# Kernel optimization log

Hardware: AMD Instinct MI355X
Metric: run time of the kernel (lower is better)

## Reference

```python
import jax, jax.numpy as jnp
import numpy as np

B, C, N = 4, 64, 512
H = 128  # hidden width; MLP input is 2*C = 128


def setup_inputs() -> dict:
    key = jax.random.key(0)
    k0, k1, k2 = jax.random.split(key, 3)
    x = jax.random.normal(k0, (B, C, N), dtype=jnp.float32)
    # Torch Linear init ~ U(-1/sqrt(fan_in), 1/sqrt(fan_in)); stored as (in, out) for einsum.
    W1 = jax.random.normal(k1, (2 * C, H), dtype=jnp.float32) * (1.0 / np.sqrt(2 * C))
    b1 = jnp.zeros((H,), dtype=jnp.float32)
    W2 = jax.random.normal(k2, (H, 1), dtype=jnp.float32) * (1.0 / np.sqrt(H))
    b2 = jnp.zeros((1,), dtype=jnp.float32)
    return {"x": x, "W1": W1, "b1": b1, "W2": W2, "b2": b2}


def reference(x, W1, b1, W2, b2):
    # x: (B, C, N). Equivalent to the per-offset loop: for every pair (i, j) with
    # j > i, score = MLP(concat(x[:, :, i], x[:, :, j])), placed at y[:, i, j].
    # Dropout is identity in eval mode.
    b, c, n = x.shape
    xt = jnp.transpose(x, (0, 2, 1))                      # (B, N, C)
    left = jnp.broadcast_to(xt[:, :, None, :], (b, n, n, c))   # row index i
    right = jnp.broadcast_to(xt[:, None, :, :], (b, n, n, c))  # col index j
    pairs = jnp.concatenate([left, right], axis=-1)       # (B, N, N, 2C)
    h = jax.nn.relu(jnp.einsum('bijc,ch->bijh', pairs, W1) + b1)
    score = (jnp.einsum('bijh,ho->bijo', h, W2) + b2)[..., 0]  # (B, N, N)
    mask = jnp.triu(jnp.ones((n, n), dtype=score.dtype), k=1)  # strict upper triangle
    return score * mask
```

## Files before the change

kernel.cpp:

```cpp
#include <hip/hip_runtime.h>

#define B_ 4
#define C_ 64
#define N_ 512
#define H_ 128

__global__ __launch_bounds__(256) void proj_kernel(
    const float* __restrict__ x, const float* __restrict__ W1,
    const float* __restrict__ b1, float* __restrict__ Lbuf,
    float* __restrict__ Rbuf)
{
    __shared__ float Wl[64 * 128];
    __shared__ float xs[16 * 68];

    const int t    = threadIdx.x;
    const int half = blockIdx.x >> 7;
    const int rem  = blockIdx.x & 127;
    const int b    = rem >> 5;
    const int i0   = (rem & 31) * 16;
    const int cbase = half * 64;

    const float4* W14 = (const float4*)W1;
    float4* Wl4 = (float4*)Wl;
    #pragma unroll
    for (int k = 0; k < 8; ++k)
        Wl4[t + k * 256] = W14[cbase * 32 + t + k * 256];

    #pragma unroll
    for (int k = 0; k < 4; ++k) {
        int idx = t + k * 256;
        int c = idx >> 4, ii = idx & 15;
        xs[ii * 68 + c] = x[b * (C_ * N_) + c * N_ + i0 + ii];
    }
    __syncthreads();

    const int hq  = t & 31;
    const int il  = (t >> 5) * 2;
    const int col = hq * 4;

    float4 a0, a1;
    if (half) { a0 = *(const float4*)(b1 + col); a1 = a0; }
    else      { a0 = make_float4(0.f, 0.f, 0.f, 0.f); a1 = a0; }

    #pragma unroll
    for (int c = 0; c < 64; c += 4) {
        float4 xv0 = *(float4*)(xs + il * 68 + c);
        float4 xv1 = *(float4*)(xs + (il + 1) * 68 + c);
        const float* x0p = (const float*)&xv0;
        const float* x1p = (const float*)&xv1;
        #pragma unroll
        for (int cc = 0; cc < 4; ++cc) {
            float4 w = Wl4[(c + cc) * 32 + hq];
            a0.x = fmaf(w.x, x0p[cc], a0.x);
            a0.y = fmaf(w.y, x0p[cc], a0.y);
            a0.z = fmaf(w.z, x0p[cc], a0.z);
            a0.w = fmaf(w.w, x0p[cc], a0.w);
            a1.x = fmaf(w.x, x1p[cc], a1.x);
            a1.y = fmaf(w.y, x1p[cc], a1.y);
            a1.z = fmaf(w.z, x1p[cc], a1.z);
            a1.w = fmaf(w.w, x1p[cc], a1.w);
        }
    }

    float* buf = half ? Rbuf : Lbuf;
    float* o = buf + b * (N_ * H_) + (i0 + il) * H_ + col;
    *(float4*)o = a0;
    *(float4*)(o + H_) = a1;
}

__global__ __launch_bounds__(256) void pair_kernel(
    const float* __restrict__ Lbuf, const float* __restrict__ Rbuf,
    const float* __restrict__ W2, const float* __restrict__ b2,
    float* __restrict__ out)
{
    __shared__ float Lt[64 * 128];
    __shared__ float Rt[64 * 128];

    const int t    = threadIdx.x;
    const int b    = blockIdx.x >> 6;
    const int tile = blockIdx.x & 63;
    const int ti0  = (tile >> 3) * 64;
    const int tj0  = (tile & 7) * 64;

    float* outb = out + b * (N_ * N_);

    if (tj0 < ti0) {
        float4 z = make_float4(0.f, 0.f, 0.f, 0.f);
        #pragma unroll
        for (int k = 0; k < 4; ++k) {
            int idx4 = t + k * 256;
            int r = idx4 >> 4, cc = idx4 & 15;
            *(float4*)(outb + (ti0 + r) * N_ + tj0 + cc * 4) = z;
        }
        return;
    }

    float4* Lt4 = (float4*)Lt;
    float4* Rt4 = (float4*)Rt;
    #pragma unroll
    for (int k = 0; k < 8; ++k) {
        int idx4 = t + k * 256;
        int row = idx4 >> 5, hc = idx4 & 31;
        float4 lv = *(const float4*)(Lbuf + b * (N_ * H_) + (ti0 + row) * H_ + hc * 4);
        float4 rv = *(const float4*)(Rbuf + b * (N_ * H_) + (tj0 + row) * H_ + hc * 4);
        int sc = (hc + (row >> 2)) & 31;
        Lt4[row * 32 + sc] = lv;
        Rt4[row * 32 + sc] = rv;
    }
    __syncthreads();

    const int w    = t >> 6;
    const int lane = t & 63;
    const int wi   = (w >> 1) * 32, wj = (w & 1) * 32;
    const int til  = wi + ((lane >> 3) & 7) * 4;
    const int tjl  = wj + (lane & 7) * 4;
    const int rotL = til >> 2;
    const int rotR = tjl >> 2;

    float acc[4][4];
    #pragma unroll
    for (int r = 0; r < 4; ++r)
        #pragma unroll
        for (int c = 0; c < 4; ++c) acc[r][c] = 0.f;

    #pragma unroll 2
    for (int hc = 0; hc < 32; ++hc) {
        const int scL = (hc + rotL) & 31;
        const int scR = (hc + rotR) & 31;
        float4 Lr[4], Rc[4];
        #pragma unroll
        for (int r = 0; r < 4; ++r) Lr[r] = Lt4[(til + r) * 32 + scL];
        #pragma unroll
        for (int c = 0; c < 4; ++c) Rc[c] = Rt4[(tjl + c) * 32 + scR];
        float4 wv = *(const float4*)(W2 + hc * 4);
        const float* wp = (const float*)&wv;
        #pragma unroll
        for (int r = 0; r < 4; ++r) {
            const float* lp = (const float*)&Lr[r];
            #pragma unroll
            for (int c = 0; c < 4; ++c) {
                const float* rp = (const float*)&Rc[c];
                float s = acc[r][c];
                #pragma unroll
                for (int k = 0; k < 4; ++k) {
                    float v = fmaxf(lp[k] + rp[k], 0.f);
                    s = fmaf(v, wp[k], s);
                }
                acc[r][c] = s;
            }
        }
    }

    const float bias2 = b2[0];
    #pragma unroll
    for (int r = 0; r < 4; ++r) {
        const int gi = ti0 + til + r;
        float4 v;
        float* vp = (float*)&v;
        #pragma unroll
        for (int c = 0; c < 4; ++c) {
            const int gj = tj0 + tjl + c;
            vp[c] = (gj > gi) ? (acc[r][c] + bias2) : 0.f;
        }
        *(float4*)(outb + gi * N_ + tj0 + tjl) = v;
    }
}

extern "C" void kernel_launch(void* const* d_in, const int* in_sizes, int n_in,
                              void* d_out, int out_size, void* d_ws, size_t ws_size,
                              hipStream_t stream)
{
    const float* x  = (const float*)d_in[0];
    const float* W1 = (const float*)d_in[1];
    const float* b1 = (const float*)d_in[2];
    const float* W2 = (const float*)d_in[3];
    const float* b2 = (const float*)d_in[4];
    float* out  = (float*)d_out;
    float* Lbuf = (float*)d_ws;
    float* Rbuf = Lbuf + B_ * N_ * H_;

    proj_kernel<<<256, 256, 0, stream>>>(x, W1, b1, Lbuf, Rbuf);
    pair_kernel<<<B_ * 64, 256, 0, stream>>>(Lbuf, Rbuf, W2, b2, out);
}
```

Measured before the change: 80.41 us.

## Shrink pair kernel tiles to 32x32 with one-wave blocks and XOR swizzle

```diff
diff --git a/kernel.cpp b/kernel.cpp
--- a/kernel.cpp
+++ b/kernel.cpp
@@ -68,54 +68,48 @@
     *(float4*)(o + H_) = a1;
 }
 
-__global__ __launch_bounds__(256) void pair_kernel(
+__global__ __launch_bounds__(64) void pair_kernel(
     const float* __restrict__ Lbuf, const float* __restrict__ Rbuf,
     const float* __restrict__ W2, const float* __restrict__ b2,
     float* __restrict__ out)
 {
-    __shared__ float Lt[64 * 128];
-    __shared__ float Rt[64 * 128];
+    __shared__ float4 Lt4[32 * 32];
+    __shared__ float4 Rt4[32 * 32];
 
     const int t    = threadIdx.x;
-    const int b    = blockIdx.x >> 6;
-    const int tile = blockIdx.x & 63;
-    const int ti0  = (tile >> 3) * 64;
-    const int tj0  = (tile & 7) * 64;
+    const int b    = blockIdx.x >> 8;
+    const int tile = blockIdx.x & 255;
+    const int ti0  = (tile >> 4) * 32;
+    const int tj0  = (tile & 15) * 32;
 
     float* outb = out + b * (N_ * N_);
 
-    if (tj0 < ti0) {
+    if (tj0 + 31 <= ti0) {
         float4 z = make_float4(0.f, 0.f, 0.f, 0.f);
         #pragma unroll
         for (int k = 0; k < 4; ++k) {
-            int idx4 = t + k * 256;
-            int r = idx4 >> 4, cc = idx4 & 15;
-            *(float4*)(outb + (ti0 + r) * N_ + tj0 + cc * 4) = z;
+            int idx = t + k * 64;
+            int r = idx >> 3, cq = idx & 7;
+            *(float4*)(outb + (ti0 + r) * N_ + tj0 + cq * 4) = z;
         }
         return;
     }
 
-    float4* Lt4 = (float4*)Lt;
-    float4* Rt4 = (float4*)Rt;
+    const float* Lsrc = Lbuf + b * (N_ * H_) + ti0 * H_;
+    const float* Rsrc = Rbuf + b * (N_ * H_) + tj0 * H_;
     #pragma unroll
-    for (int k = 0; k < 8; ++k) {
-        int idx4 = t + k * 256;
-        int row = idx4 >> 5, hc = idx4 & 31;
-        float4 lv = *(const float4*)(Lbuf + b * (N_ * H_) + (ti0 + row) * H_ + hc * 4);
-        float4 rv = *(const float4*)(Rbuf + b * (N_ * H_) + (tj0 + row) * H_ + hc * 4);
-        int sc = (hc + (row >> 2)) & 31;
-        Lt4[row * 32 + sc] = lv;
-        Rt4[row * 32 + sc] = rv;
+    for (int k = 0; k < 16; ++k) {
+        int idx = t + k * 64;
+        int row = idx >> 5, hc = idx & 31;
+        int sc = hc ^ (row >> 2);
+        Lt4[row * 32 + sc] = *(const float4*)(Lsrc + idx * 4);
+        Rt4[row * 32 + sc] = *(const float4*)(Rsrc + idx * 4);
     }
     __syncthreads();
 
-    const int w    = t >> 6;
-    const int lane = t & 63;
-    const int wi   = (w >> 1) * 32, wj = (w & 1) * 32;
-    const int til  = wi + ((lane >> 3) & 7) * 4;
-    const int tjl  = wj + (lane & 7) * 4;
-    const int rotL = til >> 2;
-    const int rotR = tjl >> 2;
+    const int gL  = t >> 3;
+    const int gR  = t & 7;
+    const int til = gL * 4, tjl = gR * 4;
 
     float acc[4][4];
     #pragma unroll
@@ -123,16 +117,18 @@
         #pragma unroll
         for (int c = 0; c < 4; ++c) acc[r][c] = 0.f;
 
+    const float4* W24 = (const float4*)W2;
+
     #pragma unroll 2
     for (int hc = 0; hc < 32; ++hc) {
-        const int scL = (hc + rotL) & 31;
-        const int scR = (hc + rotR) & 31;
+        const int scL = hc ^ gL;
+        const int scR = hc ^ gR;
         float4 Lr[4], Rc[4];
         #pragma unroll
         for (int r = 0; r < 4; ++r) Lr[r] = Lt4[(til + r) * 32 + scL];
         #pragma unroll
         for (int c = 0; c < 4; ++c) Rc[c] = Rt4[(tjl + c) * 32 + scR];
-        float4 wv = *(const float4*)(W2 + hc * 4);
+        float4 wv = W24[hc];
         const float* wp = (const float*)&wv;
         #pragma unroll
         for (int r = 0; r < 4; ++r) {
@@ -180,5 +176,5 @@
     float* Rbuf = Lbuf + B_ * N_ * H_;
 
     proj_kernel<<<256, 256, 0, stream>>>(x, W1, b1, Lbuf, Rbuf);
-    pair_kernel<<<B_ * 64, 256, 0, stream>>>(Lbuf, Rbuf, W2, b2, out);
+    pair_kernel<<<B_ * 256, 64, 0, stream>>>(Lbuf, Rbuf, W2, b2, out);
 }
```

New measurement: 81.39 us. About the same (+1.2%).
